# Kernel tuning notes

Measured on AMD Instinct MI355X. Metric: run time of the kernel, lower is better.

Reference implementation:

```python
import jax, jax.numpy as jnp
import numpy as np

L, D, H, DFF, V, NB = 8, 1024, 16, 4096, 50257, 2048
HD = D // H
B, T = 2, 2048
EPS = 1e-5


def setup_inputs() -> dict:
    key = jax.random.key(0)
    ks = jax.random.split(key, 10)
    s = 0.02
    return {
        "x": jax.random.randint(ks[0], (B, T), 0, V),
        "W_emb": jax.random.normal(ks[1], (V, D), jnp.float32) * s,  # tied tok_emb / out_head
        "pos_emb": jax.random.normal(ks[2], (NB, D), jnp.float32) * s,
        "Wq": jax.random.normal(ks[3], (L, D, D), jnp.float32) * s,
        "Wk": jax.random.normal(ks[4], (L, D, D), jnp.float32) * s,
        "Wv": jax.random.normal(ks[5], (L, D, D), jnp.float32) * s,
        "Wo": jax.random.normal(ks[6], (L, D, D), jnp.float32) * s,
        "bo": jnp.zeros((L, D), jnp.float32),
        "n1_scale": jnp.ones((L, D), jnp.float32),
        "n1_shift": jnp.zeros((L, D), jnp.float32),
        "n2_scale": jnp.ones((L, D), jnp.float32),
        "n2_shift": jnp.zeros((L, D), jnp.float32),
        "W1": jax.random.normal(ks[7], (L, DFF, D), jnp.float32) * s,
        "b1": jnp.zeros((L, DFF), jnp.float32),
        "W2": jax.random.normal(ks[8], (L, D, DFF), jnp.float32) * s,
        "b2": jnp.zeros((L, D), jnp.float32),
        "f_scale": jnp.ones((D,), jnp.float32),
        "f_shift": jnp.zeros((D,), jnp.float32),
    }


def layernorm(x, scale, shift):
    # Matches custom LayerNorm: uses sample std (ddof=1) and (std + eps) in denominator
    mean = jnp.mean(x, axis=-1, keepdims=True)
    std = jnp.std(x, axis=-1, keepdims=True, ddof=1)
    return scale * ((x - mean) / (std + EPS)) + shift


def gelu(x):
    c = jnp.sqrt(jnp.asarray(2.0 / jnp.pi, x.dtype))
    return 0.5 * x * (1.0 + jnp.tanh(c * (x + 0.044715 * x * x * x)))


def reference(x, W_emb, pos_emb, Wq, Wk, Wv, Wo, bo,
              n1_scale, n1_shift, n2_scale, n2_shift,
              W1, b1, W2, b2, f_scale, f_shift):
    b, t = x.shape
    h = W_emb[x] + pos_emb[:t]  # [B,T,D]
    causal = jnp.triu(jnp.ones((t, t), dtype=bool), 1)  # True above diagonal => masked
    scale = jnp.sqrt(jnp.asarray(HD, h.dtype))
    neg_inf = jnp.asarray(-jnp.inf, h.dtype)
    for l in range(L):
        xn = layernorm(h, n1_scale[l], n1_shift[l])
        q = (xn @ Wq[l].T).reshape(b, t, H, HD).transpose(0, 2, 1, 3)  # [B,H,T,hd]
        k = (xn @ Wk[l].T).reshape(b, t, H, HD).transpose(0, 2, 1, 3)
        v = (xn @ Wv[l].T).reshape(b, t, H, HD).transpose(0, 2, 1, 3)
        scores = jnp.einsum('bhqd,bhkd->bhqk', q, k)
        scores = jnp.where(causal, neg_inf, scores) / scale  # mask then scale, as in source
        aw = jax.nn.softmax(scores, axis=-1)
        ctx = jnp.einsum('bhqk,bhkd->bhqd', aw, v)
        ctx = ctx.transpose(0, 2, 1, 3).reshape(b, t, D)
        h = h + (ctx @ Wo[l].T + bo[l])
        xn2 = layernorm(h, n2_scale[l], n2_shift[l])
        h = h + (gelu(xn2 @ W1[l].T + b1[l]) @ W2[l].T + b2[l])
    h = layernorm(h, f_scale, f_shift)
    logits = h[:, -1:, :] @ W_emb.T  # last-token logits [B,1,V] (targets=None path)
    return logits
```

## Files before the change

### kernel.cpp

```cpp
#include <hip/hip_runtime.h>
#include <math.h>

#define L_   8
#define D_   1024
#define H_   16
#define HD_  64
#define DFF_ 4096
#define V_   50257
#define T_   2048
#define B_   2
#define M_   (B_*T_)

typedef __attribute__((ext_vector_type(8))) short short8;
typedef __attribute__((ext_vector_type(4))) float f4;
typedef __attribute__((ext_vector_type(4))) unsigned short us4;

#define GLOAD16(gp, lp) \
  __builtin_amdgcn_global_load_lds((__attribute__((address_space(1))) void*)(gp), \
                                   (__attribute__((address_space(3))) void*)(lp), 16, 0, 0)

__device__ __forceinline__ unsigned short f2bf(float f) {
  union { float f; unsigned u; } c; c.f = f;
  return (unsigned short)((c.u + 0x7fffu + ((c.u >> 16) & 1u)) >> 16);
}

__global__ __launch_bounds__(256) void cvt_kernel(const float* __restrict__ s,
                                                  unsigned short* __restrict__ d, int n) {
  int i = (blockIdx.x * 256 + threadIdx.x) * 4;
  const int stride = gridDim.x * 256 * 4;
  for (; i < n; i += stride) {
    f4 f = *(const f4*)(s + i);
    us4 o;
    o.x = f2bf(f.x); o.y = f2bf(f.y); o.z = f2bf(f.z); o.w = f2bf(f.w);
    *(us4*)(d + i) = o;
  }
}

__global__ __launch_bounds__(256) void embed_kernel(const int* __restrict__ x,
    const float* __restrict__ wemb, const float* __restrict__ pos, float* __restrict__ h) {
  const int m = blockIdx.x;
  const int t = m & (T_ - 1);
  const int idx = x[m];
  const int d = threadIdx.x * 4;
  f4 a = *(const f4*)(wemb + (size_t)idx * D_ + d);
  f4 b = *(const f4*)(pos + (size_t)t * D_ + d);
  a = a + b;
  *(f4*)(h + (size_t)m * D_ + d) = a;
}

__global__ __launch_bounds__(256) void ln_kernel(const float* __restrict__ h,
    const float* __restrict__ sc, const float* __restrict__ sh,
    unsigned short* __restrict__ out) {
  const int row = blockIdx.x, tid = threadIdx.x;
  f4 x = *(const f4*)(h + (size_t)row * D_ + tid * 4);
  float s1 = x.x + x.y + x.z + x.w;
  float s2 = x.x * x.x + x.y * x.y + x.z * x.z + x.w * x.w;
#pragma unroll
  for (int off = 32; off > 0; off >>= 1) {
    s1 += __shfl_down(s1, off);
    s2 += __shfl_down(s2, off);
  }
  __shared__ float r1[4], r2[4];
  if ((tid & 63) == 0) { r1[tid >> 6] = s1; r2[tid >> 6] = s2; }
  __syncthreads();
  float t1 = r1[0] + r1[1] + r1[2] + r1[3];
  float t2 = r2[0] + r2[1] + r2[2] + r2[3];
  float mean = t1 * (1.0f / D_);
  float var = fmaxf((t2 - t1 * mean) * (1.0f / (D_ - 1)), 0.0f);
  float inv = 1.0f / (sqrtf(var) + 1e-5f);
  f4 s = *(const f4*)(sc + tid * 4);
  f4 b = *(const f4*)(sh + tid * 4);
  us4 o;
  o.x = f2bf(s.x * ((x.x - mean) * inv) + b.x);
  o.y = f2bf(s.y * ((x.y - mean) * inv) + b.y);
  o.z = f2bf(s.z * ((x.z - mean) * inv) + b.z);
  o.w = f2bf(s.w * ((x.w - mean) * inv) + b.w);
  *(us4*)(out + (size_t)row * D_ + tid * 4) = o;
}

__global__ __launch_bounds__(256) void ln_final_kernel(const float* __restrict__ h,
    const float* __restrict__ sc, const float* __restrict__ sh, float* __restrict__ out) {
  const int b = blockIdx.x, tid = threadIdx.x;
  const int row = b * T_ + (T_ - 1);
  f4 x = *(const f4*)(h + (size_t)row * D_ + tid * 4);
  float s1 = x.x + x.y + x.z + x.w;
  float s2 = x.x * x.x + x.y * x.y + x.z * x.z + x.w * x.w;
#pragma unroll
  for (int off = 32; off > 0; off >>= 1) {
    s1 += __shfl_down(s1, off);
    s2 += __shfl_down(s2, off);
  }
  __shared__ float r1[4], r2[4];
  if ((tid & 63) == 0) { r1[tid >> 6] = s1; r2[tid >> 6] = s2; }
  __syncthreads();
  float t1 = r1[0] + r1[1] + r1[2] + r1[3];
  float t2 = r2[0] + r2[1] + r2[2] + r2[3];
  float mean = t1 * (1.0f / D_);
  float var = fmaxf((t2 - t1 * mean) * (1.0f / (D_ - 1)), 0.0f);
  float inv = 1.0f / (sqrtf(var) + 1e-5f);
  f4 s = *(const f4*)(sc + tid * 4);
  f4 bb = *(const f4*)(sh + tid * 4);
  f4 o;
  o.x = s.x * ((x.x - mean) * inv) + bb.x;
  o.y = s.y * ((x.y - mean) * inv) + bb.y;
  o.z = s.z * ((x.z - mean) * inv) + bb.z;
  o.w = s.w * ((x.w - mean) * inv) + bb.w;
  *(f4*)(out + (size_t)b * D_ + tid * 4) = o;
}

#define EP_QKV 0
#define EP_RES 1
#define EP_GELU 2

template <int MODE>
__global__ __launch_bounds__(256) void gemm_kernel(
    const unsigned short* __restrict__ A,
    const unsigned short* __restrict__ Bq,
    const unsigned short* __restrict__ Bk,
    const unsigned short* __restrict__ Bv,
    const float* __restrict__ bias,
    float* __restrict__ hres,
    unsigned short* __restrict__ out0,
    unsigned short* __restrict__ out1,
    unsigned short* __restrict__ out2,
    int N, int K) {
  __shared__ __attribute__((aligned(16))) unsigned short As[128 * 32];
  __shared__ __attribute__((aligned(16))) unsigned short Bs[128 * 32];
  const int tid = threadIdx.x;
  const int wv = tid >> 6, lane = tid & 63;
  const int quad = lane >> 4, l16 = lane & 15;
  const int bm0 = blockIdx.x * 128;
  int bn0;
  const unsigned short* Bw;
  unsigned short* qout = out0;
  if (MODE == EP_QKV) {
    int sel = blockIdx.y >> 3;
    bn0 = (blockIdx.y & 7) * 128;
    Bw = (sel == 0) ? Bq : ((sel == 1) ? Bk : Bv);
    qout = (sel == 0) ? out0 : ((sel == 1) ? out1 : out2);
  } else {
    bn0 = blockIdx.y * 128;
    Bw = Bq;
  }
  const int wm = (wv & 1) * 64, wn = (wv >> 1) * 64;

  f4 acc[4][4] = {};

  for (int k0 = 0; k0 < K; k0 += 32) {
#pragma unroll
    for (int i = 0; i < 2; i++) {
      int c = i * 256 + tid;
      int row = c >> 2;
      int c4 = (c & 3) ^ (row & 3);
      GLOAD16(A + (size_t)(bm0 + row) * K + k0 + c4 * 8,
              (char*)As + (i * 256 + wv * 64) * 16);
      GLOAD16(Bw + (size_t)(bn0 + row) * K + k0 + c4 * 8,
              (char*)Bs + (i * 256 + wv * 64) * 16);
    }
    __syncthreads();
    short8 af[4], bfr[4];
#pragma unroll
    for (int mt = 0; mt < 4; mt++) {
      int row = wm + mt * 16 + l16;
      af[mt] = *(const short8*)(As + row * 32 + ((quad ^ (row & 3)) * 8));
    }
#pragma unroll
    for (int nt = 0; nt < 4; nt++) {
      int row = wn + nt * 16 + l16;
      bfr[nt] = *(const short8*)(Bs + row * 32 + ((quad ^ (row & 3)) * 8));
    }
#pragma unroll
    for (int mt = 0; mt < 4; mt++)
#pragma unroll
      for (int nt = 0; nt < 4; nt++)
        acc[mt][nt] = __builtin_amdgcn_mfma_f32_16x16x32_bf16(af[mt], bfr[nt], acc[mt][nt], 0, 0, 0);
    __syncthreads();
  }

#pragma unroll
  for (int mt = 0; mt < 4; mt++) {
#pragma unroll
    for (int nt = 0; nt < 4; nt++) {
#pragma unroll
      for (int r = 0; r < 4; r++) {
        int gm = bm0 + wm + mt * 16 + quad * 4 + r;
        int gn = bn0 + wn + nt * 16 + l16;
        float val = acc[mt][nt][r];
        if (MODE == EP_QKV) {
          int b = gm >> 11, t = gm & (T_ - 1);
          int hh = gn >> 6, hd = gn & 63;
          qout[(size_t)((b * H_ + hh) * T_ + t) * HD_ + hd] = f2bf(val);
        } else if (MODE == EP_RES) {
          size_t idx = (size_t)gm * D_ + gn;
          hres[idx] += val + bias[gn];
        } else {
          float xg = val + bias[gn];
          float z = 0.7978845608028654f * (xg + 0.044715f * xg * xg * xg);
          float e = __expf(2.0f * z);
          float th = 1.0f - 2.0f / (e + 1.0f);
          out0[(size_t)gm * DFF_ + gn] = f2bf(0.5f * xg * (1.0f + th));
        }
      }
    }
  }
}

__global__ __launch_bounds__(256) void vtrans_kernel(const unsigned short* __restrict__ v,
                                                     unsigned short* __restrict__ vt) {
  __shared__ __attribute__((aligned(16))) unsigned short tile[64 * 72];
  const int tid = threadIdx.x;
  const int t0 = blockIdx.x * 64;
  const size_t bh = (size_t)(blockIdx.z * H_ + blockIdx.y);
  const unsigned short* vp = v + bh * T_ * HD_;
#pragma unroll
  for (int i = 0; i < 2; i++) {
    int c = i * 256 + tid;
    int row = c >> 3, c8 = c & 7;
    *(short8*)(tile + row * 72 + c8 * 8) =
        *(const short8*)(vp + (size_t)(t0 + row) * HD_ + c8 * 8);
  }
  __syncthreads();
  unsigned short* op = vt + bh * (size_t)HD_ * T_;
#pragma unroll
  for (int i = 0; i < 2; i++) {
    int c = i * 256 + tid;
    int drow = c >> 3, c8 = c & 7;
    short8 o;
#pragma unroll
    for (int j = 0; j < 8; j++) o[j] = (short)tile[(c8 * 8 + j) * 72 + drow];
    *(short8*)(op + (size_t)drow * T_ + t0 + c8 * 8) = o;
  }
}

__global__ __launch_bounds__(256) void attn_kernel(
    const unsigned short* __restrict__ q,
    const unsigned short* __restrict__ k,
    const unsigned short* __restrict__ vt,
    unsigned short* __restrict__ ctx) {
  __shared__ __attribute__((aligned(16))) unsigned short Ks[64 * 64];
  __shared__ __attribute__((aligned(16))) unsigned short Vs[64 * 64];
  __shared__ __attribute__((aligned(16))) unsigned short Ps[4][16 * 88];
  const int tid = threadIdx.x;
  const int wv = tid >> 6, lane = tid & 63;
  const int quad = lane >> 4, l16 = lane & 15;
  const int qt = blockIdx.x, hh = blockIdx.y, b = blockIdx.z;
  const size_t bh = (size_t)(b * H_ + hh);
  const unsigned short* qp = q + bh * T_ * HD_;
  const unsigned short* kp = k + bh * T_ * HD_;
  const unsigned short* vp = vt + bh * (size_t)HD_ * T_;

  const int qrow = qt * 64 + wv * 16 + l16;
  const short8 qf0 = *(const short8*)(qp + (size_t)qrow * HD_ + quad * 8);
  const short8 qf1 = *(const short8*)(qp + (size_t)qrow * HD_ + 32 + quad * 8);

  f4 of[4] = {};
  float mrow[4] = {-1e30f, -1e30f, -1e30f, -1e30f};
  float lrow[4] = {0.f, 0.f, 0.f, 0.f};
  unsigned short* pw = Ps[wv];

  const int nkt = qt + 1;
  for (int kt = 0; kt < nkt; kt++) {
    const int kb = kt * 64;
#pragma unroll
    for (int i = 0; i < 2; i++) {
      int c = i * 256 + tid;
      int row = c >> 3;
      int c8 = (c & 7) ^ (row & 7);
      GLOAD16(kp + (size_t)(kb + row) * HD_ + c8 * 8, (char*)Ks + (i * 256 + wv * 64) * 16);
      GLOAD16(vp + (size_t)row * T_ + kb + c8 * 8, (char*)Vs + (i * 256 + wv * 64) * 16);
    }
    __syncthreads();
    float sv[4][4];
#pragma unroll
    for (int nt = 0; nt < 4; nt++) {
      int row = nt * 16 + l16;
      int p0 = (quad ^ (row & 7)) * 8;
      int p1 = ((4 + quad) ^ (row & 7)) * 8;
      short8 kf0 = *(const short8*)(Ks + row * 64 + p0);
      short8 kf1 = *(const short8*)(Ks + row * 64 + p1);
      f4 z = {};
      z = __builtin_amdgcn_mfma_f32_16x16x32_bf16(qf0, kf0, z, 0, 0, 0);
      z = __builtin_amdgcn_mfma_f32_16x16x32_bf16(qf1, kf1, z, 0, 0, 0);
#pragma unroll
      for (int r = 0; r < 4; r++) {
        float s = z[r] * 0.125f;
        if (kt == qt) {
          int col = kb + nt * 16 + l16;
          int rowg = qt * 64 + wv * 16 + quad * 4 + r;
          if (col > rowg) s = -1e30f;
        }
        sv[nt][r] = s;
      }
    }
    float mnew[4], alpha[4];
#pragma unroll
    for (int r = 0; r < 4; r++) {
      float mx = fmaxf(fmaxf(sv[0][r], sv[1][r]), fmaxf(sv[2][r], sv[3][r]));
      mx = fmaxf(mx, __shfl_xor(mx, 1));
      mx = fmaxf(mx, __shfl_xor(mx, 2));
      mx = fmaxf(mx, __shfl_xor(mx, 4));
      mx = fmaxf(mx, __shfl_xor(mx, 8));
      mnew[r] = fmaxf(mrow[r], mx);
      alpha[r] = __expf(mrow[r] - mnew[r]);
      mrow[r] = mnew[r];
    }
    float pv[4][4];
#pragma unroll
    for (int nt = 0; nt < 4; nt++)
#pragma unroll
      for (int r = 0; r < 4; r++)
        pv[nt][r] = __expf(sv[nt][r] - mnew[r]);
#pragma unroll
    for (int r = 0; r < 4; r++) {
      float s = pv[0][r] + pv[1][r] + pv[2][r] + pv[3][r];
      s += __shfl_xor(s, 1);
      s += __shfl_xor(s, 2);
      s += __shfl_xor(s, 4);
      s += __shfl_xor(s, 8);
      lrow[r] = lrow[r] * alpha[r] + s;
    }
#pragma unroll
    for (int nt = 0; nt < 4; nt++) {
      of[nt][0] *= alpha[0];
      of[nt][1] *= alpha[1];
      of[nt][2] *= alpha[2];
      of[nt][3] *= alpha[3];
    }
#pragma unroll
    for (int nt = 0; nt < 4; nt++)
#pragma unroll
      for (int r = 0; r < 4; r++)
        pw[(quad * 4 + r) * 88 + nt * 16 + l16] = f2bf(pv[nt][r]);
    short8 pf0 = *(const short8*)(pw + l16 * 88 + quad * 8);
    short8 pf1 = *(const short8*)(pw + l16 * 88 + 32 + quad * 8);
#pragma unroll
    for (int nt = 0; nt < 4; nt++) {
      int row = nt * 16 + l16;
      int p0 = (quad ^ (row & 7)) * 8;
      int p1 = ((4 + quad) ^ (row & 7)) * 8;
      short8 vf0 = *(const short8*)(Vs + row * 64 + p0);
      short8 vf1 = *(const short8*)(Vs + row * 64 + p1);
      of[nt] = __builtin_amdgcn_mfma_f32_16x16x32_bf16(pf0, vf0, of[nt], 0, 0, 0);
      of[nt] = __builtin_amdgcn_mfma_f32_16x16x32_bf16(pf1, vf1, of[nt], 0, 0, 0);
    }
    __syncthreads();
  }
#pragma unroll
  for (int nt = 0; nt < 4; nt++) {
#pragma unroll
    for (int r = 0; r < 4; r++) {
      int rowg = qt * 64 + wv * 16 + quad * 4 + r;
      int dcol = hh * HD_ + nt * 16 + l16;
      ctx[(size_t)(b * T_ + rowg) * D_ + dcol] = f2bf(of[nt][r] / lrow[r]);
    }
  }
}

__global__ __launch_bounds__(256) void logits_kernel(const float* __restrict__ wemb,
    const float* __restrict__ hln, float* __restrict__ out) {
  const int tid = threadIdx.x;
  const int wv = tid >> 6, lane = tid & 63;
  const int rbase = blockIdx.x * 32 + wv * 8;
  f4 h0[4], h1[4];
#pragma unroll
  for (int j = 0; j < 4; j++) {
    h0[j] = *(const f4*)(hln + j * 256 + lane * 4);
    h1[j] = *(const f4*)(hln + D_ + j * 256 + lane * 4);
  }
#pragma unroll
  for (int i = 0; i < 8; i++) {
    int r = rbase + i;
    if (r >= V_) return;
    const float* wr = wemb + (size_t)r * D_;
    float a0 = 0.f, a1 = 0.f;
#pragma unroll
    for (int j = 0; j < 4; j++) {
      f4 w4 = *(const f4*)(wr + j * 256 + lane * 4);
      a0 += w4.x * h0[j].x + w4.y * h0[j].y + w4.z * h0[j].z + w4.w * h0[j].w;
      a1 += w4.x * h1[j].x + w4.y * h1[j].y + w4.z * h1[j].z + w4.w * h1[j].w;
    }
#pragma unroll
    for (int off = 32; off > 0; off >>= 1) {
      a0 += __shfl_down(a0, off);
      a1 += __shfl_down(a1, off);
    }
    if (lane == 0) {
      out[r] = a0;
      out[V_ + r] = a1;
    }
  }
}

extern "C" void kernel_launch(void* const* d_in, const int* in_sizes, int n_in,
                              void* d_out, int out_size, void* d_ws, size_t ws_size,
                              hipStream_t stream) {
  (void)in_sizes; (void)n_in; (void)out_size; (void)ws_size;
  const int*   x    = (const int*)  d_in[0];
  const float* Wemb = (const float*)d_in[1];
  const float* pos  = (const float*)d_in[2];
  const float* Wq   = (const float*)d_in[3];
  const float* Wk   = (const float*)d_in[4];
  const float* Wv   = (const float*)d_in[5];
  const float* Wo   = (const float*)d_in[6];
  const float* bo   = (const float*)d_in[7];
  const float* n1s  = (const float*)d_in[8];
  const float* n1b  = (const float*)d_in[9];
  const float* n2s  = (const float*)d_in[10];
  const float* n2b  = (const float*)d_in[11];
  const float* W1   = (const float*)d_in[12];
  const float* b1   = (const float*)d_in[13];
  const float* W2   = (const float*)d_in[14];
  const float* b2   = (const float*)d_in[15];
  const float* fsc  = (const float*)d_in[16];
  const float* fsh  = (const float*)d_in[17];
  float* out = (float*)d_out;

  char* p = (char*)d_ws;
  auto alloc = [&](size_t bytes) -> char* {
    char* r = p;
    p += (bytes + 255) & ~(size_t)255;
    return r;
  };
  unsigned short* wq_b = (unsigned short*)alloc((size_t)L_ * D_ * D_ * 2);
  unsigned short* wk_b = (unsigned short*)alloc((size_t)L_ * D_ * D_ * 2);
  unsigned short* wv_b = (unsigned short*)alloc((size_t)L_ * D_ * D_ * 2);
  unsigned short* wo_b = (unsigned short*)alloc((size_t)L_ * D_ * D_ * 2);
  unsigned short* w1_b = (unsigned short*)alloc((size_t)L_ * DFF_ * D_ * 2);
  unsigned short* w2_b = (unsigned short*)alloc((size_t)L_ * DFF_ * D_ * 2);
  float*          h    = (float*)alloc((size_t)M_ * D_ * 4);
  unsigned short* xn   = (unsigned short*)alloc((size_t)M_ * D_ * 2);
  unsigned short* qb   = (unsigned short*)alloc((size_t)M_ * D_ * 2);
  unsigned short* kb   = (unsigned short*)alloc((size_t)M_ * D_ * 2);
  unsigned short* vb   = (unsigned short*)alloc((size_t)M_ * D_ * 2);
  unsigned short* vtb  = (unsigned short*)alloc((size_t)M_ * D_ * 2);
  unsigned short* ctx  = (unsigned short*)alloc((size_t)M_ * D_ * 2);
  unsigned short* act  = (unsigned short*)alloc((size_t)M_ * DFF_ * 2);
  float*          hln  = (float*)alloc(2 * D_ * 4);

  cvt_kernel<<<2048, 256, 0, stream>>>(Wq, wq_b, L_ * D_ * D_);
  cvt_kernel<<<2048, 256, 0, stream>>>(Wk, wk_b, L_ * D_ * D_);
  cvt_kernel<<<2048, 256, 0, stream>>>(Wv, wv_b, L_ * D_ * D_);
  cvt_kernel<<<2048, 256, 0, stream>>>(Wo, wo_b, L_ * D_ * D_);
  cvt_kernel<<<2048, 256, 0, stream>>>(W1, w1_b, L_ * DFF_ * D_);
  cvt_kernel<<<2048, 256, 0, stream>>>(W2, w2_b, L_ * DFF_ * D_);
  embed_kernel<<<M_, 256, 0, stream>>>(x, Wemb, pos, h);

  for (int l = 0; l < L_; l++) {
    ln_kernel<<<M_, 256, 0, stream>>>(h, n1s + l * D_, n1b + l * D_, xn);
    gemm_kernel<EP_QKV><<<dim3(32, 24), 256, 0, stream>>>(
        xn, wq_b + (size_t)l * D_ * D_, wk_b + (size_t)l * D_ * D_,
        wv_b + (size_t)l * D_ * D_, nullptr, nullptr, qb, kb, vb, D_, D_);
    vtrans_kernel<<<dim3(32, H_, B_), 256, 0, stream>>>(vb, vtb);
    attn_kernel<<<dim3(32, H_, B_), 256, 0, stream>>>(qb, kb, vtb, ctx);
    gemm_kernel<EP_RES><<<dim3(32, 8), 256, 0, stream>>>(
        ctx, wo_b + (size_t)l * D_ * D_, nullptr, nullptr,
        bo + l * D_, h, nullptr, nullptr, nullptr, D_, D_);
    ln_kernel<<<M_, 256, 0, stream>>>(h, n2s + l * D_, n2b + l * D_, xn);
    gemm_kernel<EP_GELU><<<dim3(32, 32), 256, 0, stream>>>(
        xn, w1_b + (size_t)l * DFF_ * D_, nullptr, nullptr,
        b1 + l * DFF_, nullptr, act, nullptr, nullptr, DFF_, D_);
    gemm_kernel<EP_RES><<<dim3(32, 8), 256, 0, stream>>>(
        act, w2_b + (size_t)l * DFF_ * D_, nullptr, nullptr,
        b2 + l * D_, h, nullptr, nullptr, nullptr, D_, DFF_);
  }
  ln_final_kernel<<<2, 256, 0, stream>>>(h, fsc, fsh, hln);
  logits_kernel<<<(V_ + 31) / 32, 256, 0, stream>>>(Wemb, hln, out);
}
```

Baseline: 3.658 ms.

## Split-K residual GEMMs folded into LayerNorm; rewrite attention without online max

```diff
diff --git a/kernel.cpp b/kernel.cpp
--- a/kernel.cpp
+++ b/kernel.cpp
@@ -18,6 +18,8 @@
 #define GLOAD16(gp, lp) \
   __builtin_amdgcn_global_load_lds((__attribute__((address_space(1))) void*)(gp), \
                                    (__attribute__((address_space(3))) void*)(lp), 16, 0, 0)
+
+#define MFMA(a, b, c) __builtin_amdgcn_mfma_f32_16x16x32_bf16((a), (b), (c), 0, 0, 0)
 
 __device__ __forceinline__ unsigned short f2bf(float f) {
   union { float f; unsigned u; } c; c.f = f;
@@ -48,11 +50,8 @@
   *(f4*)(h + (size_t)m * D_ + d) = a;
 }
 
-__global__ __launch_bounds__(256) void ln_kernel(const float* __restrict__ h,
-    const float* __restrict__ sc, const float* __restrict__ sh,
-    unsigned short* __restrict__ out) {
-  const int row = blockIdx.x, tid = threadIdx.x;
-  f4 x = *(const f4*)(h + (size_t)row * D_ + tid * 4);
+__device__ __forceinline__ void ln_core(f4 x, const float* sc, const float* sh,
+                                        int tid, unsigned short* outp) {
   float s1 = x.x + x.y + x.z + x.w;
   float s2 = x.x * x.x + x.y * x.y + x.z * x.z + x.w * x.w;
 #pragma unroll
@@ -75,14 +74,41 @@
   o.y = f2bf(s.y * ((x.y - mean) * inv) + b.y);
   o.z = f2bf(s.z * ((x.z - mean) * inv) + b.z);
   o.w = f2bf(s.w * ((x.w - mean) * inv) + b.w);
-  *(us4*)(out + (size_t)row * D_ + tid * 4) = o;
+  *(us4*)outp = o;
+}
+
+__global__ __launch_bounds__(256) void ln_kernel(const float* __restrict__ h,
+    const float* __restrict__ sc, const float* __restrict__ sh,
+    unsigned short* __restrict__ out) {
+  const int row = blockIdx.x, tid = threadIdx.x;
+  f4 x = *(const f4*)(h + (size_t)row * D_ + tid * 4);
+  ln_core(x, sc, sh, tid, out + (size_t)row * D_ + tid * 4);
+}
+
+__global__ __launch_bounds__(256) void ln_fold_kernel(float* __restrict__ h,
+    const float* __restrict__ part,
+    const float* __restrict__ sc, const float* __restrict__ sh,
+    unsigned short* __restrict__ out) {
+  const int row = blockIdx.x, tid = threadIdx.x;
+  const size_t o = (size_t)row * D_ + tid * 4;
+  f4 x = *(const f4*)(h + o);
+  f4 p0 = *(const f4*)(part + o);
+  f4 p1 = *(const f4*)(part + (size_t)M_ * D_ + o);
+  x = x + p0 + p1;
+  *(f4*)(h + o) = x;
+  ln_core(x, sc, sh, tid, out + o);
 }
 
 __global__ __launch_bounds__(256) void ln_final_kernel(const float* __restrict__ h,
+    const float* __restrict__ part,
     const float* __restrict__ sc, const float* __restrict__ sh, float* __restrict__ out) {
   const int b = blockIdx.x, tid = threadIdx.x;
-  const int row = b * T_ + (T_ - 1);
-  f4 x = *(const f4*)(h + (size_t)row * D_ + tid * 4);
+  const size_t row = (size_t)b * T_ + (T_ - 1);
+  const size_t o = row * D_ + tid * 4;
+  f4 x = *(const f4*)(h + o);
+  f4 p0 = *(const f4*)(part + o);
+  f4 p1 = *(const f4*)(part + (size_t)M_ * D_ + o);
+  x = x + p0 + p1;
   float s1 = x.x + x.y + x.z + x.w;
   float s2 = x.x * x.x + x.y * x.y + x.z * x.z + x.w * x.w;
 #pragma unroll
@@ -100,16 +126,16 @@
   float inv = 1.0f / (sqrtf(var) + 1e-5f);
   f4 s = *(const f4*)(sc + tid * 4);
   f4 bb = *(const f4*)(sh + tid * 4);
-  f4 o;
-  o.x = s.x * ((x.x - mean) * inv) + bb.x;
-  o.y = s.y * ((x.y - mean) * inv) + bb.y;
-  o.z = s.z * ((x.z - mean) * inv) + bb.z;
-  o.w = s.w * ((x.w - mean) * inv) + bb.w;
-  *(f4*)(out + (size_t)b * D_ + tid * 4) = o;
+  f4 oo;
+  oo.x = s.x * ((x.x - mean) * inv) + bb.x;
+  oo.y = s.y * ((x.y - mean) * inv) + bb.y;
+  oo.z = s.z * ((x.z - mean) * inv) + bb.z;
+  oo.w = s.w * ((x.w - mean) * inv) + bb.w;
+  *(f4*)(out + (size_t)b * D_ + tid * 4) = oo;
 }
 
 #define EP_QKV 0
-#define EP_RES 1
+#define EP_PART 1
 #define EP_GELU 2
 
 template <int MODE>
@@ -119,7 +145,7 @@
     const unsigned short* __restrict__ Bk,
     const unsigned short* __restrict__ Bv,
     const float* __restrict__ bias,
-    float* __restrict__ hres,
+    float* __restrict__ part,
     unsigned short* __restrict__ out0,
     unsigned short* __restrict__ out1,
     unsigned short* __restrict__ out2,
@@ -144,9 +170,12 @@
   }
   const int wm = (wv & 1) * 64, wn = (wv >> 1) * 64;
 
+  int kbeg = 0, kend = K;
+  if (MODE == EP_PART) { int kh = K >> 1; kbeg = blockIdx.z * kh; kend = kbeg + kh; }
+
   f4 acc[4][4] = {};
 
-  for (int k0 = 0; k0 < K; k0 += 32) {
+  for (int k0 = kbeg; k0 < kend; k0 += 32) {
 #pragma unroll
     for (int i = 0; i < 2; i++) {
       int c = i * 256 + tid;
@@ -173,7 +202,7 @@
     for (int mt = 0; mt < 4; mt++)
 #pragma unroll
       for (int nt = 0; nt < 4; nt++)
-        acc[mt][nt] = __builtin_amdgcn_mfma_f32_16x16x32_bf16(af[mt], bfr[nt], acc[mt][nt], 0, 0, 0);
+        acc[mt][nt] = MFMA(af[mt], bfr[nt], acc[mt][nt]);
     __syncthreads();
   }
 
@@ -190,9 +219,9 @@
           int b = gm >> 11, t = gm & (T_ - 1);
           int hh = gn >> 6, hd = gn & 63;
           qout[(size_t)((b * H_ + hh) * T_ + t) * HD_ + hd] = f2bf(val);
-        } else if (MODE == EP_RES) {
-          size_t idx = (size_t)gm * D_ + gn;
-          hres[idx] += val + bias[gn];
+        } else if (MODE == EP_PART) {
+          size_t idx = ((size_t)blockIdx.z * M_ + gm) * D_ + gn;
+          part[idx] = val + (blockIdx.z == 0 ? bias[gn] : 0.0f);
         } else {
           float xg = val + bias[gn];
           float z = 0.7978845608028654f * (xg + 0.044715f * xg * xg * xg);
@@ -237,122 +266,89 @@
     const unsigned short* __restrict__ k,
     const unsigned short* __restrict__ vt,
     unsigned short* __restrict__ ctx) {
-  __shared__ __attribute__((aligned(16))) unsigned short Ks[64 * 64];
-  __shared__ __attribute__((aligned(16))) unsigned short Vs[64 * 64];
-  __shared__ __attribute__((aligned(16))) unsigned short Ps[4][16 * 88];
+  __shared__ __attribute__((aligned(16))) unsigned short Ps[4][16 * 68];
   const int tid = threadIdx.x;
   const int wv = tid >> 6, lane = tid & 63;
   const int quad = lane >> 4, l16 = lane & 15;
-  const int qt = blockIdx.x, hh = blockIdx.y, b = blockIdx.z;
+  const int qt = (int)gridDim.x - 1 - (int)blockIdx.x;
+  const int hh = blockIdx.y, b = blockIdx.z;
   const size_t bh = (size_t)(b * H_ + hh);
-  const unsigned short* qp = q + bh * T_ * HD_;
-  const unsigned short* kp = k + bh * T_ * HD_;
+  const unsigned short* qp = q + bh * (size_t)T_ * HD_;
+  const unsigned short* kp = k + bh * (size_t)T_ * HD_;
   const unsigned short* vp = vt + bh * (size_t)HD_ * T_;
 
-  const int qrow = qt * 64 + wv * 16 + l16;
-  const short8 qf0 = *(const short8*)(qp + (size_t)qrow * HD_ + quad * 8);
-  const short8 qf1 = *(const short8*)(qp + (size_t)qrow * HD_ + 32 + quad * 8);
+  const int qrow0 = qt * 64 + wv * 16;
+  const short8 qf0 = *(const short8*)(qp + (size_t)(qrow0 + l16) * HD_ + quad * 8);
+  const short8 qf1 = *(const short8*)(qp + (size_t)(qrow0 + l16) * HD_ + 32 + quad * 8);
 
   f4 of[4] = {};
-  float mrow[4] = {-1e30f, -1e30f, -1e30f, -1e30f};
-  float lrow[4] = {0.f, 0.f, 0.f, 0.f};
+  f4 lacc = {};
+  short8 ones;
+#pragma unroll
+  for (int j = 0; j < 8; j++) ones[j] = (short)0x3F80;
+
   unsigned short* pw = Ps[wv];
-
   const int nkt = qt + 1;
+
+  short8 kf[8];
+#pragma unroll
+  for (int nt = 0; nt < 4; nt++) {
+    kf[nt * 2 + 0] = *(const short8*)(kp + (size_t)(nt * 16 + l16) * HD_ + quad * 8);
+    kf[nt * 2 + 1] = *(const short8*)(kp + (size_t)(nt * 16 + l16) * HD_ + 32 + quad * 8);
+  }
+
   for (int kt = 0; kt < nkt; kt++) {
     const int kb = kt * 64;
-#pragma unroll
-    for (int i = 0; i < 2; i++) {
-      int c = i * 256 + tid;
-      int row = c >> 3;
-      int c8 = (c & 7) ^ (row & 7);
-      GLOAD16(kp + (size_t)(kb + row) * HD_ + c8 * 8, (char*)Ks + (i * 256 + wv * 64) * 16);
-      GLOAD16(vp + (size_t)row * T_ + kb + c8 * 8, (char*)Vs + (i * 256 + wv * 64) * 16);
-    }
-    __syncthreads();
-    float sv[4][4];
+    short8 vf[8];
 #pragma unroll
     for (int nt = 0; nt < 4; nt++) {
-      int row = nt * 16 + l16;
-      int p0 = (quad ^ (row & 7)) * 8;
-      int p1 = ((4 + quad) ^ (row & 7)) * 8;
-      short8 kf0 = *(const short8*)(Ks + row * 64 + p0);
-      short8 kf1 = *(const short8*)(Ks + row * 64 + p1);
+      vf[nt * 2 + 0] = *(const short8*)(vp + (size_t)(nt * 16 + l16) * T_ + kb + quad * 8);
+      vf[nt * 2 + 1] = *(const short8*)(vp + (size_t)(nt * 16 + l16) * T_ + kb + 32 + quad * 8);
+    }
+    short8 kn[8];
+    if (kt + 1 < nkt) {
+#pragma unroll
+      for (int nt = 0; nt < 4; nt++) {
+        kn[nt * 2 + 0] = *(const short8*)(kp + (size_t)(kb + 64 + nt * 16 + l16) * HD_ + quad * 8);
+        kn[nt * 2 + 1] = *(const short8*)(kp + (size_t)(kb + 64 + nt * 16 + l16) * HD_ + 32 + quad * 8);
+      }
+    }
+    const bool last = (kt == nkt - 1);
+#pragma unroll
+    for (int nt = 0; nt < 4; nt++) {
       f4 z = {};
-      z = __builtin_amdgcn_mfma_f32_16x16x32_bf16(qf0, kf0, z, 0, 0, 0);
-      z = __builtin_amdgcn_mfma_f32_16x16x32_bf16(qf1, kf1, z, 0, 0, 0);
+      z = MFMA(qf0, kf[nt * 2 + 0], z);
+      z = MFMA(qf1, kf[nt * 2 + 1], z);
 #pragma unroll
       for (int r = 0; r < 4; r++) {
-        float s = z[r] * 0.125f;
-        if (kt == qt) {
+        float s = fminf(z[r] * 0.125f, 60.0f);
+        if (last) {
           int col = kb + nt * 16 + l16;
-          int rowg = qt * 64 + wv * 16 + quad * 4 + r;
+          int rowg = qrow0 + quad * 4 + r;
           if (col > rowg) s = -1e30f;
         }
-        sv[nt][r] = s;
+        pw[(quad * 4 + r) * 68 + nt * 16 + l16] = f2bf(__expf(s));
       }
     }
-    float mnew[4], alpha[4];
-#pragma unroll
-    for (int r = 0; r < 4; r++) {
-      float mx = fmaxf(fmaxf(sv[0][r], sv[1][r]), fmaxf(sv[2][r], sv[3][r]));
-      mx = fmaxf(mx, __shfl_xor(mx, 1));
-      mx = fmaxf(mx, __shfl_xor(mx, 2));
-      mx = fmaxf(mx, __shfl_xor(mx, 4));
-      mx = fmaxf(mx, __shfl_xor(mx, 8));
-      mnew[r] = fmaxf(mrow[r], mx);
-      alpha[r] = __expf(mrow[r] - mnew[r]);
-      mrow[r] = mnew[r];
-    }
-    float pv[4][4];
+#pragma unroll
+    for (int ks = 0; ks < 2; ks++) {
+      short8 pf = *(const short8*)(pw + l16 * 68 + ks * 32 + quad * 8);
+      lacc = MFMA(pf, ones, lacc);
+#pragma unroll
+      for (int nt = 0; nt < 4; nt++)
+        of[nt] = MFMA(pf, vf[nt * 2 + ks], of[nt]);
+    }
+#pragma unroll
+    for (int j = 0; j < 8; j++) kf[j] = kn[j];
+  }
+
+#pragma unroll
+  for (int r = 0; r < 4; r++) {
+    float inv = 1.0f / lacc[r];
+    int rowg = qrow0 + quad * 4 + r;
 #pragma unroll
     for (int nt = 0; nt < 4; nt++)
-#pragma unroll
-      for (int r = 0; r < 4; r++)
-        pv[nt][r] = __expf(sv[nt][r] - mnew[r]);
-#pragma unroll
-    for (int r = 0; r < 4; r++) {
-      float s = pv[0][r] + pv[1][r] + pv[2][r] + pv[3][r];
-      s += __shfl_xor(s, 1);
-      s += __shfl_xor(s, 2);
-      s += __shfl_xor(s, 4);
-      s += __shfl_xor(s, 8);
-      lrow[r] = lrow[r] * alpha[r] + s;
-    }
-#pragma unroll
-    for (int nt = 0; nt < 4; nt++) {
-      of[nt][0] *= alpha[0];
-      of[nt][1] *= alpha[1];
-      of[nt][2] *= alpha[2];
-      of[nt][3] *= alpha[3];
-    }
-#pragma unroll
-    for (int nt = 0; nt < 4; nt++)
-#pragma unroll
-      for (int r = 0; r < 4; r++)
-        pw[(quad * 4 + r) * 88 + nt * 16 + l16] = f2bf(pv[nt][r]);
-    short8 pf0 = *(const short8*)(pw + l16 * 88 + quad * 8);
-    short8 pf1 = *(const short8*)(pw + l16 * 88 + 32 + quad * 8);
-#pragma unroll
-    for (int nt = 0; nt < 4; nt++) {
-      int row = nt * 16 + l16;
-      int p0 = (quad ^ (row & 7)) * 8;
-      int p1 = ((4 + quad) ^ (row & 7)) * 8;
-      short8 vf0 = *(const short8*)(Vs + row * 64 + p0);
-      short8 vf1 = *(const short8*)(Vs + row * 64 + p1);
-      of[nt] = __builtin_amdgcn_mfma_f32_16x16x32_bf16(pf0, vf0, of[nt], 0, 0, 0);
-      of[nt] = __builtin_amdgcn_mfma_f32_16x16x32_bf16(pf1, vf1, of[nt], 0, 0, 0);
-    }
-    __syncthreads();
-  }
-#pragma unroll
-  for (int nt = 0; nt < 4; nt++) {
-#pragma unroll
-    for (int r = 0; r < 4; r++) {
-      int rowg = qt * 64 + wv * 16 + quad * 4 + r;
-      int dcol = hh * HD_ + nt * 16 + l16;
-      ctx[(size_t)(b * T_ + rowg) * D_ + dcol] = f2bf(of[nt][r] / lrow[r]);
-    }
+      ctx[(size_t)(b * T_ + rowg) * D_ + hh * HD_ + nt * 16 + l16] = f2bf(of[nt][r] * inv);
   }
 }
 
@@ -436,6 +432,7 @@
   unsigned short* ctx  = (unsigned short*)alloc((size_t)M_ * D_ * 2);
   unsigned short* act  = (unsigned short*)alloc((size_t)M_ * DFF_ * 2);
   float*          hln  = (float*)alloc(2 * D_ * 4);
+  float* part = (float*)qb;
 
   cvt_kernel<<<2048, 256, 0, stream>>>(Wq, wq_b, L_ * D_ * D_);
   cvt_kernel<<<2048, 256, 0, stream>>>(Wk, wk_b, L_ * D_ * D_);
@@ -446,23 +443,26 @@
   embed_kernel<<<M_, 256, 0, stream>>>(x, Wemb, pos, h);
 
   for (int l = 0; l < L_; l++) {
-    ln_kernel<<<M_, 256, 0, stream>>>(h, n1s + l * D_, n1b + l * D_, xn);
+    if (l == 0)
+      ln_kernel<<<M_, 256, 0, stream>>>(h, n1s, n1b, xn);
+    else
+      ln_fold_kernel<<<M_, 256, 0, stream>>>(h, part, n1s + l * D_, n1b + l * D_, xn);
     gemm_kernel<EP_QKV><<<dim3(32, 24), 256, 0, stream>>>(
         xn, wq_b + (size_t)l * D_ * D_, wk_b + (size_t)l * D_ * D_,
         wv_b + (size_t)l * D_ * D_, nullptr, nullptr, qb, kb, vb, D_, D_);
     vtrans_kernel<<<dim3(32, H_, B_), 256, 0, stream>>>(vb, vtb);
     attn_kernel<<<dim3(32, H_, B_), 256, 0, stream>>>(qb, kb, vtb, ctx);
-    gemm_kernel<EP_RES><<<dim3(32, 8), 256, 0, stream>>>(
+    gemm_kernel<EP_PART><<<dim3(32, 8, 2), 256, 0, stream>>>(
         ctx, wo_b + (size_t)l * D_ * D_, nullptr, nullptr,
-        bo + l * D_, h, nullptr, nullptr, nullptr, D_, D_);
-    ln_kernel<<<M_, 256, 0, stream>>>(h, n2s + l * D_, n2b + l * D_, xn);
+        bo + l * D_, part, nullptr, nullptr, nullptr, D_, D_);
+    ln_fold_kernel<<<M_, 256, 0, stream>>>(h, part, n2s + l * D_, n2b + l * D_, xn);
     gemm_kernel<EP_GELU><<<dim3(32, 32), 256, 0, stream>>>(
         xn, w1_b + (size_t)l * DFF_ * D_, nullptr, nullptr,
         b1 + l * DFF_, nullptr, act, nullptr, nullptr, DFF_, D_);
-    gemm_kernel<EP_RES><<<dim3(32, 8), 256, 0, stream>>>(
+    gemm_kernel<EP_PART><<<dim3(32, 8, 2), 256, 0, stream>>>(
         act, w2_b + (size_t)l * DFF_ * D_, nullptr, nullptr,
-        b2 + l * D_, h, nullptr, nullptr, nullptr, D_, DFF_);
-  }
-  ln_final_kernel<<<2, 256, 0, stream>>>(h, fsc, fsh, hln);
+        b2 + l * D_, part, nullptr, nullptr, nullptr, D_, DFF_);
+  }
+  ln_final_kernel<<<2, 256, 0, stream>>>(h, part, fsc, fsh, hln);
   logits_kernel<<<(V_ + 31) / 32, 256, 0, stream>>>(Wemb, hln, out);
 }
```

Result: slower. 4.486 ms (+22.6%).
